# Performance work log

Hardware: AMD Instinct MI355X
Metric: run time of the kernel (lower is better)

## Reference

```python
import jax, jax.numpy as jnp
import numpy as np

N = 100000   # nodes
E = 1600000  # edges
F = 64       # num_features
H = 64       # hidden_units
C = 10       # num_classes
G = 1000     # graphs in batch
BN_EPS = 1e-5


def setup_inputs() -> dict:
    key = jax.random.key(0)
    ks = jax.random.split(key, 32)
    inp = {
        "x": jax.random.normal(ks[0], (N, F), dtype=jnp.float32),
        "edge_index": jax.random.randint(ks[1], (2, E), 0, N, dtype=jnp.int64),
        "batch": jnp.sort(jax.random.randint(ks[2], (N,), 0, G, dtype=jnp.int64)),
    }
    i = 3
    def w(shape, scale):
        nonlocal i
        a = jax.random.normal(ks[i], shape, dtype=jnp.float32) * scale
        i += 1
        return a
    for l, din in [(0, F), (1, H)]:
        inp[f"c{l}_w1"] = w((din, H), 1.0 / np.sqrt(din))
        inp[f"c{l}_b1"] = jnp.zeros((H,), jnp.float32)
        inp[f"c{l}_g1"] = jnp.ones((H,), jnp.float32)
        inp[f"c{l}_be1"] = jnp.zeros((H,), jnp.float32)
        inp[f"c{l}_w2"] = w((H, H), 1.0 / np.sqrt(H))
        inp[f"c{l}_b2"] = jnp.zeros((H,), jnp.float32)
        inp[f"bn{l}_g"] = jnp.ones((H,), jnp.float32)
        inp[f"bn{l}_b"] = jnp.zeros((H,), jnp.float32)
    for l, din in [(0, F), (1, H), (2, H)]:
        inp[f"l{l}_w"] = w((din, C), 1.0 / np.sqrt(din))
        inp[f"l{l}_b"] = jnp.zeros((C,), jnp.float32)
    return inp


def _bn(h, g, b):
    # BatchNorm1d in training mode: batch statistics over node axis
    m = jnp.mean(h, axis=0)
    v = jnp.var(h, axis=0)
    return g * (h - m) * jax.lax.rsqrt(v + BN_EPS) + b


def _gin_conv(h, src, dst, w1, b1, g1, be1, w2, b2):
    # scatter-add neighbor aggregation: out[dst] += h[src]; eps = 0
    agg = jax.ops.segment_sum(h[src], dst, num_segments=N)
    z = h + agg                      # (1 + eps) * x + sum_j x_j
    z = jax.nn.relu(_bn(z @ w1 + b1, g1, be1))
    return z @ w2 + b2


def reference(x, edge_index, batch,
              c0_w1, c0_b1, c0_g1, c0_be1, c0_w2, c0_b2, bn0_g, bn0_b,
              c1_w1, c1_b1, c1_g1, c1_be1, c1_w2, c1_b2, bn1_g, bn1_b,
              l0_w, l0_b, l1_w, l1_b, l2_w, l2_b):
    src, dst = edge_index[0], edge_index[1]
    h0 = x
    h1 = jax.nn.relu(_bn(_gin_conv(h0, src, dst, c0_w1, c0_b1, c0_g1, c0_be1, c0_w2, c0_b2), bn0_g, bn0_b))
    h2 = jax.nn.relu(_bn(_gin_conv(h1, src, dst, c1_w1, c1_b1, c1_g1, c1_be1, c1_w2, c1_b2), bn1_g, bn1_b))
    # jumping-knowledge readout: per-layer global_add_pool -> Linear -> sum (dropout=0)
    out = jnp.zeros((G, C), dtype=x.dtype)
    for h, w, b in [(h0, l0_w, l0_b), (h1, l1_w, l1_b), (h2, l2_w, l2_b)]:
        pooled = jax.ops.segment_sum(h, batch, num_segments=G)
        out = out + pooled @ w + b
    return out
```

## Files before the change

### kernel.cpp

```cpp
#include <hip/hip_runtime.h>
#include <hip/hip_bf16.h>

#define BN_EPS 1e-5f
#define NBMAX 512
#define CHUNK 4096
#define CAP   5120
#define PCAP  9216

typedef __hip_bfloat16 bf16;
typedef __attribute__((ext_vector_type(8))) short short8;
typedef __attribute__((ext_vector_type(4))) float f32x4;

__device__ __forceinline__ float b2f(bf16 v) { return __bfloat162float(v); }
__device__ __forceinline__ bf16 f2b(float v) { return __float2bfloat16(v); }
__device__ __forceinline__ float bl(unsigned u) { return __uint_as_float(u << 16); }
__device__ __forceinline__ float bh(unsigned u) { return __uint_as_float(u & 0xffff0000u); }
__device__ __forceinline__ unsigned pack2(float x, float y) {
    union { bf16 b[2]; unsigned u; } p;
    p.b[0] = f2b(x); p.b[1] = f2b(y);
    return p.u;
}
__device__ __forceinline__ float bs2f(short s) {
    return __uint_as_float(((unsigned)(unsigned short)s) << 16);
}
__device__ __forceinline__ short f2bs(float v) {
    bf16 b = f2b(v);
    return *reinterpret_cast<short*>(&b);
}

__global__ __launch_bounds__(256) void initcast_k(
    const float* __restrict__ in, bf16* __restrict__ out, int n4, int total4,
    int* __restrict__ bcur, int NB)
{
    if (blockIdx.x == 0) {
        for (int i = threadIdx.x; i < NB; i += 256) bcur[i] = i * CAP;
    }
    int i = blockIdx.x * 256 + threadIdx.x;
    if (i >= total4) return;
    if (i < n4) {
        float4 v = ((const float4*)in)[i];
        union { ushort4 u; bf16 b[4]; } p;
        p.b[0] = f2b(v.x); p.b[1] = f2b(v.y); p.b[2] = f2b(v.z); p.b[3] = f2b(v.w);
        ((ushort4*)out)[i] = p.u;
    } else {
        ushort4 z; z.x = 0; z.y = 0; z.z = 0; z.w = 0;
        ((ushort4*)out)[i] = z;
    }
}

__global__ __launch_bounds__(256) void binscatter_k(
    const int* __restrict__ src, const int* __restrict__ dst,
    int* __restrict__ bcur, int* __restrict__ tmp, int E, int NB)
{
    __shared__ int hist[NBMAX];
    __shared__ int loff[NBMAX];
    __shared__ int gb[NBMAX];
    __shared__ int lcur[NBMAX];
    __shared__ int staged[CHUNK];
    __shared__ unsigned short sb[CHUNK];
    __shared__ int ssc[256];
    const int t = threadIdx.x;
    for (int i = t; i < NB; i += 256) { hist[i] = 0; lcur[i] = 0; }
    __syncthreads();
    const int base = blockIdx.x * CHUNK;
    const int lim = min(CHUNK, E - base);
    int myb[16], myw[16];
    int cnt = 0;
    for (int i = t; i < lim; i += 256) {
        int d = dst[base + i];
        int s_ = src[base + i];
        int b = d >> 8;
        myb[cnt] = b;
        myw[cnt] = (s_ << 8) | (d & 255);
        cnt++;
        atomicAdd(&hist[b], 1);
    }
    __syncthreads();
    int v0 = (2 * t     < NB) ? hist[2 * t]     : 0;
    int v1 = (2 * t + 1 < NB) ? hist[2 * t + 1] : 0;
    ssc[t] = v0 + v1;
    __syncthreads();
    for (int off = 1; off < 256; off <<= 1) {
        int a = (t >= off) ? ssc[t - off] : 0;
        __syncthreads();
        ssc[t] += a;
        __syncthreads();
    }
    int excl = ssc[t] - (v0 + v1);
    if (2 * t < NB)     loff[2 * t] = excl;
    if (2 * t + 1 < NB) loff[2 * t + 1] = excl + v0;
    __syncthreads();
    for (int b = t; b < NB; b += 256)
        if (hist[b] > 0) gb[b] = atomicAdd(&bcur[b], hist[b]);
    for (int i = 0; i < cnt; i++) {
        int b = myb[i];
        int p = loff[b] + atomicAdd(&lcur[b], 1);
        staged[p] = myw[i];
        sb[p] = (unsigned short)b;
    }
    __syncthreads();
    for (int i = t; i < lim; i += 256) {
        int b = sb[i];
        tmp[gb[b] + (i - loff[b])] = staged[i];
    }
}

__global__ __launch_bounds__(256) void csr_k(
    const int* __restrict__ bcur, const int* __restrict__ tmp,
    int* __restrict__ rowptr, int* __restrict__ rowend,
    int* __restrict__ adj, int N)
{
    __shared__ int hist[256], pfx[256], cur[256], ssc[256];
    __shared__ int sadj[PCAP];
    const int b = blockIdx.x, t = threadIdx.x;
    const int lo = b * CAP;
    const int plo = b * PCAP;
    const int cnt = min(bcur[b] - lo, CAP);
    hist[t] = 0; cur[t] = 0;
    __syncthreads();
    for (int i = t; i < cnt; i += 256)
        atomicAdd(&hist[tmp[lo + i] & 255], 1);
    __syncthreads();
    const int v = hist[t];
    const int pv = (v + 15) & ~15;
    ssc[t] = pv;
    __syncthreads();
    for (int off = 1; off < 256; off <<= 1) {
        int a = (t >= off) ? ssc[t - off] : 0;
        __syncthreads();
        ssc[t] += a;
        __syncthreads();
    }
    const int myp = ssc[t] - pv;
    pfx[t] = myp;
    const int node = b * 256 + t;
    if (node < N) {
        rowptr[node] = plo + myp;
        rowend[node] = plo + myp + pv;
    }
    __syncthreads();
    const int pcnt = ssc[255];
    for (int i = t; i < cnt; i += 256) {
        int w = tmp[lo + i];
        int d = w & 255;
        int p = pfx[d] + atomicAdd(&cur[d], 1);
        sadj[p] = w >> 8;
    }
    __syncthreads();
    for (int i = v; i < pv; i++) sadj[myp + i] = N;
    __syncthreads();
    for (int i = t; i < pcnt; i += 256) adj[plo + i] = sadj[i];
}

__global__ __launch_bounds__(256, 4) void aggregate_k(
    const bf16* __restrict__ h, const int* __restrict__ rowptr,
    const int* __restrict__ rowend, const int* __restrict__ adj,
    bf16* __restrict__ z, int N)
{
    const int lane = threadIdx.x & 31;
    const int n = blockIdx.x * 8 + (threadIdx.x >> 5);
    if (n >= N) return;
    const unsigned* hp = (const unsigned*)h;
    const int b = rowptr[n], e = rowend[n];

    unsigned u = hp[(size_t)n * 32 + lane];
    float s0 = bl(u), s1 = bh(u);

    for (int i = b; i < e; i += 16) {
        int m[16];
        #pragma unroll
        for (int k = 0; k < 16; k++) m[k] = adj[i + k];
        unsigned w[16];
        #pragma unroll
        for (int k = 0; k < 16; k++) w[k] = hp[(size_t)m[k] * 32 + lane];
        #pragma unroll
        for (int k = 0; k < 16; k++) {
            s0 += bl(w[k]);
            s1 += bh(w[k]);
        }
    }
    ((unsigned*)z)[(size_t)n * 32 + lane] = pack2(s0, s1);
}

__global__ __launch_bounds__(256) void ewact_k(
    const bf16* __restrict__ y, const float* __restrict__ sc,
    const float* __restrict__ sh, bf16* __restrict__ h, int N)
{
    const int idx = blockIdx.x * 256 + threadIdx.x;
    const int total = (N + 1) * 8;
    if (idx >= total) return;
    short8 v;
    if (idx < N * 8) {
        const int f0 = (idx & 7) * 8;
        v = *(const short8*)(y + (size_t)idx * 8);
        #pragma unroll
        for (int j = 0; j < 8; j++)
            v[j] = f2bs(fmaxf(fmaf(bs2f(v[j]), sc[f0 + j], sh[f0 + j]), 0.f));
    } else {
        #pragma unroll
        for (int j = 0; j < 8; j++) v[j] = 0;
    }
    *(short8*)(h + (size_t)idx * 8) = v;
}

template<int MODE>
__global__ __launch_bounds__(256) void gemm64_k(
    const bf16* __restrict__ A,
    const float* __restrict__ scin, const float* __restrict__ shin,
    const float* __restrict__ W, const float* __restrict__ bias,
    bf16* __restrict__ out, float* __restrict__ pstat, int nrows)
{
    __shared__ bf16 sWt[64][72];
    __shared__ bf16 sC[128][68];
    __shared__ float sSc[64], sSh[64], sB[64];
    __shared__ float sredS[64][17], sredQ[64][17];
    const int tid = threadIdx.x;

    if (tid < 64) {
        sB[tid] = bias[tid];
        if (MODE == 1) { sSc[tid] = scin[tid]; sSh[tid] = shin[tid]; }
    }
    for (int i = tid; i < 4096; i += 256) {
        int k = i >> 6, n = i & 63;
        sWt[n][k] = f2b(W[i]);
    }
    __syncthreads();

    const int wave = tid >> 6, lane = tid & 63;
    const int quad = lane >> 4, l16 = lane & 15;
    const int row0 = blockIdx.x * 128 + wave * 32;

    short8 a[2][2];
    #pragma unroll
    for (int rt = 0; rt < 2; rt++) {
        int r = row0 + rt * 16 + l16;
        int rr = min(r, nrows - 1);
        const bf16* arow = A + (size_t)rr * 64;
        a[rt][0] = *(const short8*)(arow + quad * 8);
        a[rt][1] = *(const short8*)(arow + 32 + quad * 8);
        if (MODE == 1) {
            #pragma unroll
            for (int j = 0; j < 8; j++) {
                int f0 = quad * 8 + j;
                a[rt][0][j] = f2bs(fmaxf(fmaf(bs2f(a[rt][0][j]), sSc[f0], sSh[f0]), 0.f));
                int f1 = 32 + f0;
                a[rt][1][j] = f2bs(fmaxf(fmaf(bs2f(a[rt][1][j]), sSc[f1], sSh[f1]), 0.f));
            }
        }
    }

    float psS[4], psQ[4];
    #pragma unroll
    for (int t = 0; t < 4; t++) { psS[t] = 0.f; psQ[t] = 0.f; }

    #pragma unroll
    for (int t = 0; t < 4; t++) {
        const int n = t * 16 + l16;
        short8 b0 = *(const short8*)&sWt[n][quad * 8];
        short8 b1 = *(const short8*)&sWt[n][32 + quad * 8];
        const float bn_ = sB[n];
        #pragma unroll
        for (int rt = 0; rt < 2; rt++) {
            f32x4 acc = {0.f, 0.f, 0.f, 0.f};
            acc = __builtin_amdgcn_mfma_f32_16x16x32_bf16(a[rt][0], b0, acc, 0, 0, 0);
            acc = __builtin_amdgcn_mfma_f32_16x16x32_bf16(a[rt][1], b1, acc, 0, 0, 0);
            #pragma unroll
            for (int reg = 0; reg < 4; reg++) {
                const int lr = wave * 32 + rt * 16 + quad * 4 + reg;
                float v = acc[reg] + bn_;
                sC[lr][n] = f2b(v);
                if (row0 + rt * 16 + quad * 4 + reg < nrows) {
                    psS[t] += v;
                    psQ[t] = fmaf(v, v, psQ[t]);
                }
            }
        }
    }

    #pragma unroll
    for (int t = 0; t < 4; t++) {
        sredS[t * 16 + l16][wave * 4 + quad] = psS[t];
        sredQ[t * 16 + l16][wave * 4 + quad] = psQ[t];
    }
    __syncthreads();

    const int gbase = blockIdx.x * 128;
    #pragma unroll
    for (int it = 0; it < 8; it++) {
        int idx = it * 256 + tid;
        int r = idx >> 4, c4 = idx & 15;
        if (gbase + r < nrows) {
            ushort4 v = *(const ushort4*)&sC[r][c4 * 4];
            *(ushort4*)(out + (size_t)(gbase + r) * 64 + c4 * 4) = v;
        }
    }

    if (tid < 128) {
        const int c = tid & 63;
        const float* p = (tid < 64) ? &sredS[c][0] : &sredQ[c][0];
        float s = 0.f;
        #pragma unroll
        for (int i = 0; i < 16; i++) s += p[i];
        pstat[(size_t)blockIdx.x * 128 + (tid < 64 ? c : 64 + c)] = s;
    }
}

__global__ __launch_bounds__(256) void bn_reduce_k(
    const float* __restrict__ pstat, int nblk,
    const float* __restrict__ g, const float* __restrict__ be, float invN,
    float* __restrict__ sc, float* __restrict__ sh)
{
    const int f = blockIdx.x;
    const int t = threadIdx.x;
    float S = 0.f, Q = 0.f;
    for (int b = t; b < nblk; b += 256) {
        S += pstat[(size_t)b * 128 + f];
        Q += pstat[(size_t)b * 128 + 64 + f];
    }
    __shared__ float rs[256], rq[256];
    rs[t] = S; rq[t] = Q;
    __syncthreads();
    for (int off = 128; off > 0; off >>= 1) {
        if (t < off) { rs[t] += rs[t + off]; rq[t] += rq[t + off]; }
        __syncthreads();
    }
    if (t == 0) {
        float m = rs[0] * invN;
        float v = rq[0] * invN - m * m;
        float s = g[f] * rsqrtf(v + BN_EPS);
        sc[f] = s;
        sh[f] = be[f] - m * s;
    }
}

__global__ __launch_bounds__(256) void pool_readout_k(
    const bf16* __restrict__ xb, const bf16* __restrict__ h1,
    const bf16* __restrict__ y1, const int* __restrict__ batch,
    const float* __restrict__ scB, const float* __restrict__ shB,
    const float* __restrict__ w0, const float* __restrict__ b0,
    const float* __restrict__ w1, const float* __restrict__ b1,
    const float* __restrict__ w2, const float* __restrict__ b2,
    float* __restrict__ out, int Nn)
{
    const int g = blockIdx.x;
    int lo = 0, hi = Nn;
    while (lo < hi) { int mid = (lo + hi) >> 1; if (batch[mid] < g) lo = mid + 1; else hi = mid; }
    const int start = lo;
    hi = Nn;
    while (lo < hi) { int mid = (lo + hi) >> 1; if (batch[mid] <= g) lo = mid + 1; else hi = mid; }
    const int end = lo;

    const int f = threadIdx.x & 63;
    const int w = threadIdx.x >> 6;
    const float sB = scB[f], tB = shB[f];

    float s0 = 0.f, s1 = 0.f, s2 = 0.f;
    for (int i = start + w; i < end; i += 4) {
        s0 += b2f(xb[(size_t)i * 64 + f]);
        s1 += b2f(h1[(size_t)i * 64 + f]);
        s2 += fmaxf(fmaf(b2f(y1[(size_t)i * 64 + f]), sB, tB), 0.f);
    }
    __shared__ float p[3][4][64];
    p[0][w][f] = s0; p[1][w][f] = s1; p[2][w][f] = s2;
    __syncthreads();
    if (threadIdx.x < 10) {
        const int c = threadIdx.x;
        float acc = b0[c] + b1[c] + b2[c];
        for (int k = 0; k < 64; k++) {
            float q0 = p[0][0][k] + p[0][1][k] + p[0][2][k] + p[0][3][k];
            float q1 = p[1][0][k] + p[1][1][k] + p[1][2][k] + p[1][3][k];
            float q2 = p[2][0][k] + p[2][1][k] + p[2][2][k] + p[2][3][k];
            acc = fmaf(q0, w0[k * 10 + c], acc);
            acc = fmaf(q1, w1[k * 10 + c], acc);
            acc = fmaf(q2, w2[k * 10 + c], acc);
        }
        out[(size_t)g * 10 + c] = acc;
    }
}

extern "C" void kernel_launch(void* const* d_in, const int* in_sizes, int n_in,
                              void* d_out, int out_size, void* d_ws, size_t ws_size,
                              hipStream_t stream)
{
    const float* x     = (const float*)d_in[0];
    const int*   edge  = (const int*)d_in[1];
    const int*   batch = (const int*)d_in[2];
    const int N = in_sizes[0] / 64;
    const int E = in_sizes[1] / 2;
    const int G = out_size / 10;
    const int* src = edge;
    const int* dst = edge + E;
    const int NB = (N + 255) / 256;

    const float* c_w1[2]  = {(const float*)d_in[3],  (const float*)d_in[11]};
    const float* c_b1[2]  = {(const float*)d_in[4],  (const float*)d_in[12]};
    const float* c_g1[2]  = {(const float*)d_in[5],  (const float*)d_in[13]};
    const float* c_be1[2] = {(const float*)d_in[6],  (const float*)d_in[14]};
    const float* c_w2[2]  = {(const float*)d_in[7],  (const float*)d_in[15]};
    const float* c_b2[2]  = {(const float*)d_in[8],  (const float*)d_in[16]};
    const float* bn_g[2]  = {(const float*)d_in[9],  (const float*)d_in[17]};
    const float* bn_b[2]  = {(const float*)d_in[10], (const float*)d_in[18]};
    const float* lw[3]    = {(const float*)d_in[19], (const float*)d_in[21], (const float*)d_in[23]};
    const float* lb[3]    = {(const float*)d_in[20], (const float*)d_in[22], (const float*)d_in[24]};

    float* out = (float*)d_out;
    const size_t nh  = (size_t)N * 64;
    const size_t nh1 = (size_t)(N + 1) * 64;
    const int PG = (N + 127) / 128;

    bf16*  zb    = (bf16*)d_ws;
    bf16*  wb    = zb + nh;
    bf16*  xb    = wb + nh;
    bf16*  hb    = xb + nh1;
    float* scsh  = (float*)(hb + nh1);
    float* pstat = scsh + 512;
    int*   rowptr = (int*)(pstat + (size_t)PG * 128);
    int*   rowend = rowptr + N;
    int*   adj    = rowend + N;
    int*   tmp    = adj + (size_t)NB * PCAP;
    int*   bcur   = tmp + (size_t)NB * CAP;

    float* sc0 = scsh;       float* sh0 = scsh + 64;
    float* scA = scsh + 128; float* shA = scsh + 192;
    float* sc2 = scsh + 256; float* sh2 = scsh + 320;
    float* scB = scsh + 384; float* shB = scsh + 448;

    const float invN = 1.0f / (float)N;
    const int binGrid  = (E + CHUNK - 1) / CHUNK;
    const int aggGrid  = (N + 7) / 8;
    const int n4       = N * 16;
    const int total4   = (N + 1) * 16;
    const int ewGrid   = (total4 + 255) / 256;
    const int actGrid  = ((N + 1) * 8 + 255) / 256;

    initcast_k<<<ewGrid, 256, 0, stream>>>(x, xb, n4, total4, bcur, NB);
    binscatter_k<<<binGrid, 256, 0, stream>>>(src, dst, bcur, tmp, E, NB);
    csr_k<<<NB, 256, 0, stream>>>(bcur, tmp, rowptr, rowend, adj, N);

    aggregate_k<<<aggGrid, 256, 0, stream>>>(xb, rowptr, rowend, adj, zb, N);
    gemm64_k<0><<<PG, 256, 0, stream>>>(zb, nullptr, nullptr,
                                        c_w1[0], c_b1[0], zb, pstat, N);
    bn_reduce_k<<<64, 256, 0, stream>>>(pstat, PG, c_g1[0], c_be1[0], invN, sc0, sh0);
    gemm64_k<1><<<PG, 256, 0, stream>>>(zb, sc0, sh0,
                                        c_w2[0], c_b2[0], zb, pstat, N);
    bn_reduce_k<<<64, 256, 0, stream>>>(pstat, PG, bn_g[0], bn_b[0], invN, scA, shA);

    ewact_k<<<actGrid, 256, 0, stream>>>(zb, scA, shA, hb, N);

    aggregate_k<<<aggGrid, 256, 0, stream>>>(hb, rowptr, rowend, adj, wb, N);
    gemm64_k<0><<<PG, 256, 0, stream>>>(wb, nullptr, nullptr,
                                        c_w1[1], c_b1[1], wb, pstat, N);
    bn_reduce_k<<<64, 256, 0, stream>>>(pstat, PG, c_g1[1], c_be1[1], invN, sc2, sh2);
    gemm64_k<1><<<PG, 256, 0, stream>>>(wb, sc2, sh2,
                                        c_w2[1], c_b2[1], wb, pstat, N);
    bn_reduce_k<<<64, 256, 0, stream>>>(pstat, PG, bn_g[1], bn_b[1], invN, scB, shB);

    pool_readout_k<<<G, 256, 0, stream>>>(xb, hb, wb, batch,
                                          scB, shB,
                                          lw[0], lb[0], lw[1], lb[1], lw[2], lb[2],
                                          out, N);
}
```

Baseline: 295.0 us.

## Use 16 lanes per node with 8-byte gathers and prefetched neighbor indices

```diff
diff --git a/kernel.cpp b/kernel.cpp
--- a/kernel.cpp
+++ b/kernel.cpp
@@ -5,7 +5,7 @@
 #define NBMAX 512
 #define CHUNK 4096
 #define CAP   5120
-#define PCAP  9216
+#define PCAP  7168
 
 typedef __hip_bfloat16 bf16;
 typedef __attribute__((ext_vector_type(8))) short short8;
@@ -122,7 +122,7 @@
         atomicAdd(&hist[tmp[lo + i] & 255], 1);
     __syncthreads();
     const int v = hist[t];
-    const int pv = (v + 15) & ~15;
+    const int pv = (v + 7) & ~7;
     ssc[t] = pv;
     __syncthreads();
     for (int off = 1; off < 256; off <<= 1) {
@@ -157,29 +157,41 @@
     const int* __restrict__ rowend, const int* __restrict__ adj,
     bf16* __restrict__ z, int N)
 {
-    const int lane = threadIdx.x & 31;
-    const int n = blockIdx.x * 8 + (threadIdx.x >> 5);
+    const int lane16 = threadIdx.x & 15;
+    const int n = blockIdx.x * 16 + (threadIdx.x >> 4);
     if (n >= N) return;
-    const unsigned* hp = (const unsigned*)h;
+    const char* hb_ = (const char*)h;
     const int b = rowptr[n], e = rowend[n];
 
-    unsigned u = hp[(size_t)n * 32 + lane];
-    float s0 = bl(u), s1 = bh(u);
-
-    for (int i = b; i < e; i += 16) {
-        int m[16];
-        #pragma unroll
-        for (int k = 0; k < 16; k++) m[k] = adj[i + k];
-        unsigned w[16];
-        #pragma unroll
-        for (int k = 0; k < 16; k++) w[k] = hp[(size_t)m[k] * 32 + lane];
-        #pragma unroll
-        for (int k = 0; k < 16; k++) {
-            s0 += bl(w[k]);
-            s1 += bh(w[k]);
-        }
-    }
-    ((unsigned*)z)[(size_t)n * 32 + lane] = pack2(s0, s1);
+    uint2 u = *(const uint2*)(hb_ + ((size_t)n << 7) + (lane16 << 3));
+    float s0 = bl(u.x), s1 = bh(u.x), s2 = bl(u.y), s3 = bh(u.y);
+
+    int m[8];
+    if (b < e) {
+        #pragma unroll
+        for (int k = 0; k < 8; k++) m[k] = adj[b + k];
+    }
+    for (int i = b; i < e; ) {
+        uint2 w[8];
+        #pragma unroll
+        for (int k = 0; k < 8; k++)
+            w[k] = *(const uint2*)(hb_ + (((size_t)(unsigned)m[k]) << 7) + (lane16 << 3));
+        const int inext = i + 8;
+        if (inext < e) {
+            #pragma unroll
+            for (int k = 0; k < 8; k++) m[k] = adj[inext + k];
+        }
+        #pragma unroll
+        for (int k = 0; k < 8; k++) {
+            s0 += bl(w[k].x); s1 += bh(w[k].x);
+            s2 += bl(w[k].y); s3 += bh(w[k].y);
+        }
+        i = inext;
+    }
+    uint2 o;
+    o.x = pack2(s0, s1);
+    o.y = pack2(s2, s3);
+    *(uint2*)((char*)z + ((size_t)n << 7) + (lane16 << 3)) = o;
 }
 
 __global__ __launch_bounds__(256) void ewact_k(
@@ -427,7 +439,7 @@
 
     const float invN = 1.0f / (float)N;
     const int binGrid  = (E + CHUNK - 1) / CHUNK;
-    const int aggGrid  = (N + 7) / 8;
+    const int aggGrid  = (N + 15) / 16;
     const int n4       = N * 16;
     const int total4   = (N + 1) * 16;
     const int ewGrid   = (total4 + 255) / 256;
```

Result: no change. 292.4 us (-0.9%).
